# Kernel tuning notes

Measured on AMD Instinct MI355X. Metric: run time of the kernel, lower is better.

## Reference

```python
import jax, jax.numpy as jnp
import numpy as np

N_FP = 235336   # n_fingerprint
N_WORD = 7844   # n_word
D = 10          # embed / hidden dim (hard-coded in module)
K = 23          # conv kernel 2*11+1
PAD = 11
N_ATOMS = 4096
L_WORDS = 65536


def setup_inputs() -> dict:
    key = jax.random.key(0)
    ks = jax.random.split(key, 16)
    s = 0.1  # weight init scale
    return {
        "fingerprints": jax.random.randint(ks[0], (N_ATOMS,), 0, N_FP),
        # scale adjacency so x + A@hs stays O(1) over 3 layers
        "adjacency": jax.random.uniform(ks[1], (N_ATOMS, N_ATOMS), dtype=jnp.float32) * (1.0 / N_ATOMS),
        "words": jax.random.randint(ks[2], (L_WORDS,), 0, N_WORD),
        "embed_fp": jax.random.normal(ks[3], (N_FP, D), dtype=jnp.float32) * s,
        "embed_word": jax.random.normal(ks[4], (N_WORD, D), dtype=jnp.float32) * s,
        "W_gnn_w": jax.random.normal(ks[5], (3, D, D), dtype=jnp.float32) * s,
        "W_gnn_b": jax.random.normal(ks[6], (3, D), dtype=jnp.float32) * s,
        "W_cnn_w": jax.random.normal(ks[7], (3, 1, 1, K, K), dtype=jnp.float32) * (s / K),
        "W_cnn_b": jax.random.normal(ks[8], (3,), dtype=jnp.float32) * s,
        "W_att_w": jax.random.normal(ks[9], (D, D), dtype=jnp.float32) * s,
        "W_att_b": jax.random.normal(ks[10], (D,), dtype=jnp.float32) * s,
        "W_out_w": jax.random.normal(ks[11], (3, 2 * D, 2 * D), dtype=jnp.float32) * s,
        "W_out_b": jax.random.normal(ks[12], (3, 2 * D), dtype=jnp.float32) * s,
        "W_int_w": jax.random.normal(ks[13], (2, 2 * D), dtype=jnp.float32) * s,
        "W_int_b": jax.random.normal(ks[14], (2,), dtype=jnp.float32) * s,
    }


def reference(fingerprints, adjacency, words, embed_fp, embed_word,
              W_gnn_w, W_gnn_b, W_cnn_w, W_cnn_b, W_att_w, W_att_b,
              W_out_w, W_out_b, W_int_w, W_int_b):
    # ---- Compound vector with GNN ----
    xs = embed_fp[fingerprints]                       # [N, D]
    for i in range(3):                                # fixed 3 layers
        hs = jax.nn.relu(xs @ W_gnn_w[i].T + W_gnn_b[i])
        xs = xs + adjacency @ hs                      # dense message passing
    compound = jnp.mean(xs, axis=0, keepdims=True)    # [1, D]

    # ---- Protein vector with attention-CNN ----
    ws = embed_word[words]                            # [L, D]
    t = ws[None, None]                                # [1,1,L,D] NCHW
    for i in range(3):
        t = jax.nn.relu(
            jax.lax.conv_general_dilated(t, W_cnn_w[i], (1, 1),
                                          [(PAD, PAD), (PAD, PAD)])
            + W_cnn_b[i])
    xs_p = t[0, 0]                                    # [L, D]

    h = jax.nn.relu(compound @ W_att_w.T + W_att_b)   # [1, D]
    hs_p = jax.nn.relu(xs_p @ W_att_w.T + W_att_b)    # [L, D]
    weights = jnp.tanh(h @ hs_p.T)                    # [1, L]
    ys = weights.T * hs_p                             # [L, D]
    protein = jnp.mean(ys, axis=0, keepdims=True)     # [1, D]

    # ---- Fusion MLP ----
    cat = jnp.concatenate([compound, protein], axis=1)  # [1, 2D]
    for j in range(3):
        cat = jax.nn.relu(cat @ W_out_w[j].T + W_out_b[j])
    return cat @ W_int_w.T + W_int_b                  # [1, 2]
```

## Files before the change

kernel.cpp:

```cpp
#include <hip/hip_runtime.h>
#include <math.h>

#define N_ATOMS 4096
#define L_WORDS 65536
#define DD 10
#define HALO 11

#define CONV_BLOCKS 256
#define CONV_BLOCK 256
#define RPW 4
#define RPB 16
#define QCOLS 1024
#define GNN_BLOCKS 1024
#define TOTAL_BLOCKS 1280
#define ATT_BLOCKS 64
#define SH_FLOATS 2926

__global__ __launch_bounds__(128) void gnn_embed(
    const int* __restrict__ fp, const float* __restrict__ embed_fp,
    const float* __restrict__ Wg, const float* __restrict__ bg,
    float* __restrict__ xs, float* __restrict__ hs)
{
    const int n = blockIdx.x * 128 + threadIdx.x;
    float x[DD];
    const float* e = embed_fp + (size_t)fp[n] * DD;
    #pragma unroll
    for (int d = 0; d < DD; ++d) x[d] = e[d];
    #pragma unroll
    for (int d = 0; d < DD; ++d) xs[d * N_ATOMS + n] = x[d];
    #pragma unroll
    for (int d = 0; d < DD; ++d) {
        float v = bg[d];
        #pragma unroll
        for (int k = 0; k < DD; ++k) v += Wg[d * DD + k] * x[k];
        hs[d * N_ATOMS + n] = fmaxf(v, 0.f);
    }
}

__global__ __launch_bounds__(128) void gnn_prep(
    const float* __restrict__ xs_in, const float* __restrict__ part,
    const float* __restrict__ Wg, const float* __restrict__ bg,
    float* __restrict__ xs_out, float* __restrict__ hs)
{
    const int n = blockIdx.x * 128 + threadIdx.x;
    float x[DD];
    #pragma unroll
    for (int d = 0; d < DD; ++d) {
        float v = xs_in[d * N_ATOMS + n];
        #pragma unroll
        for (int q = 0; q < 4; ++q)
            v += part[((size_t)q * DD + d) * N_ATOMS + n];
        x[d] = v;
        xs_out[d * N_ATOMS + n] = v;
    }
    #pragma unroll
    for (int d = 0; d < DD; ++d) {
        float v = bg[d];
        #pragma unroll
        for (int k = 0; k < DD; ++k) v += Wg[d * DD + k] * x[k];
        hs[d * N_ATOMS + n] = fmaxf(v, 0.f);
    }
}

__device__ __forceinline__ void conv_stage(
    float* sh, const int tid, const int bx,
    const float* __restrict__ tin, const int* __restrict__ words,
    const float* __restrict__ embed_word, const float* __restrict__ w,
    const float* __restrict__ bptr, float* __restrict__ tout,
    const float* __restrict__ Wa, const float* __restrict__ ba,
    float* __restrict__ hpb)
{
    const int l0 = bx * CONV_BLOCK;
    for (int idx = tid; idx < (CONV_BLOCK + 2 * HALO) * DD; idx += CONV_BLOCK) {
        int rr = idx / DD, d = idx - rr * DD;
        int gr = l0 - HALO + rr;
        float v = 0.f;
        if (gr >= 0 && gr < L_WORDS) {
            if (tin) v = tin[(size_t)gr * DD + d];
            else     v = embed_word[(size_t)words[gr] * DD + d];
        }
        sh[rr * 11 + d] = v;
    }
    __syncthreads();

    const float bias = *bptr;
    float acc[DD];
    #pragma unroll
    for (int d = 0; d < DD; ++d) acc[d] = bias;
    for (int i = 0; i < 23; ++i) {
        float row[DD];
        const float* sr = &sh[(tid + i) * 11];
        #pragma unroll
        for (int c = 0; c < DD; ++c) row[c] = sr[c];
        #pragma unroll
        for (int d = 0; d < DD; ++d) {
            #pragma unroll
            for (int c = 0; c < DD; ++c)
                acc[d] += row[c] * w[i * 23 + (c - d + 11)];
        }
    }
    const int l = l0 + tid;
    if (tout) {
        #pragma unroll
        for (int d = 0; d < DD; ++d)
            tout[(size_t)l * DD + d] = fmaxf(acc[d], 0.f);
    }
    if (hpb) {
        float xsp[DD];
        #pragma unroll
        for (int d = 0; d < DD; ++d) xsp[d] = fmaxf(acc[d], 0.f);
        #pragma unroll
        for (int d = 0; d < DD; ++d) {
            float v = ba[d];
            #pragma unroll
            for (int k = 0; k < DD; ++k) v += Wa[d * DD + k] * xsp[k];
            hpb[(size_t)l * DD + d] = fmaxf(v, 0.f);
        }
    }
}

__device__ __forceinline__ void gnn_stage(
    float* sh, const int tid, const int b,
    const float* __restrict__ hs,
    const float* __restrict__ A, float* __restrict__ part_out)
{
    const int wave = tid >> 6, lane = tid & 63;
    const int q = b & 3, rg = b >> 2;

    const int r0 = rg * RPB + wave * RPW;
    const float4* A4 = (const float4*)(A + (size_t)r0 * N_ATOMS) + q * (QCOLS / 4);
    const float4* h4 = (const float4*)hs + q * (QCOLS / 4);

    float acc[RPW][DD];
    #pragma unroll
    for (int r = 0; r < RPW; ++r)
        #pragma unroll
        for (int d = 0; d < DD; ++d) acc[r][d] = 0.f;

    #pragma unroll 1
    for (int it = 0; it < 4; ++it) {
        const int cb = it * 64 + lane;
        float4 a[RPW];
        #pragma unroll
        for (int r = 0; r < RPW; ++r) a[r] = A4[r * (N_ATOMS / 4) + cb];
        #pragma unroll
        for (int d = 0; d < DD; ++d) {
            float4 h = h4[d * (N_ATOMS / 4) + cb];
            #pragma unroll
            for (int r = 0; r < RPW; ++r) {
                acc[r][d] += a[r].x * h.x;
                acc[r][d] += a[r].y * h.y;
                acc[r][d] += a[r].z * h.z;
                acc[r][d] += a[r].w * h.w;
            }
        }
    }

    #pragma unroll
    for (int m = 1; m <= 4; m <<= 1) {
        #pragma unroll
        for (int r = 0; r < RPW; ++r)
            #pragma unroll
            for (int d = 0; d < DD; ++d)
                acc[r][d] += __shfl_xor(acc[r][d], m, 64);
    }

    if ((lane & 7) == 0) {
        const int g = lane >> 3;
        float* dst = &sh[(wave * 8 + g) * 40];
        #pragma unroll
        for (int r = 0; r < RPW; ++r)
            #pragma unroll
            for (int d = 0; d < DD; ++d) dst[r * DD + d] = acc[r][d];
    }
    __syncthreads();

    float* pdst = part_out + (size_t)q * DD * N_ATOMS + (size_t)rg * RPB;
    for (int o = tid; o < RPB * DD; o += 256) {
        const int d = o >> 4, rr = o & 15;
        const int w8 = rr >> 2, r = rr & 3;
        float v = 0.f;
        #pragma unroll
        for (int g = 0; g < 8; ++g) v += sh[(w8 * 8 + g) * 40 + r * DD + d];
        pdst[d * N_ATOMS + rr] = v;
    }
}

__global__ __launch_bounds__(256, 5) void fused_layer(
    const float* __restrict__ A, const float* __restrict__ hs,
    float* __restrict__ part_out,
    const float* __restrict__ tin, const int* __restrict__ words,
    const float* __restrict__ emb_w, const float* __restrict__ wc,
    const float* __restrict__ bc, float* __restrict__ tout,
    const float* __restrict__ Wa, const float* __restrict__ ba,
    float* __restrict__ hpb)
{
    __shared__ float sh[SH_FLOATS];
    const int tid = threadIdx.x;
    if (blockIdx.x < CONV_BLOCKS)
        conv_stage(sh, tid, blockIdx.x, tin, words, emb_w, wc, bc, tout,
                   Wa, ba, hpb);
    else
        gnn_stage(sh, tid, blockIdx.x - CONV_BLOCKS, hs, A, part_out);
}

__global__ __launch_bounds__(1024) void attn_final(
    const float* __restrict__ xs2, const float* __restrict__ part2,
    const float* __restrict__ hpb,
    const float* __restrict__ Wa, const float* __restrict__ ba,
    const float* __restrict__ Wo, const float* __restrict__ bo,
    const float* __restrict__ Wi, const float* __restrict__ bi,
    float* att_part, unsigned int* ticket, float* __restrict__ out)
{
    __shared__ float red[16][DD];
    __shared__ float shc[DD];
    __shared__ float cat[20];
    __shared__ int islast;
    const int tid = threadIdx.x, wave = tid >> 6, lane = tid & 63;

    float c[DD];
    #pragma unroll
    for (int d = 0; d < DD; ++d) c[d] = 0.f;
    #pragma unroll
    for (int s = 0; s < 4; ++s) {
        const int n = s * 1024 + tid;
        #pragma unroll
        for (int d = 0; d < DD; ++d) {
            float v = xs2[d * N_ATOMS + n];
            #pragma unroll
            for (int qq = 0; qq < 4; ++qq)
                v += part2[((size_t)qq * DD + d) * N_ATOMS + n];
            c[d] += v;
        }
    }
    #pragma unroll
    for (int m = 32; m >= 1; m >>= 1) {
        #pragma unroll
        for (int d = 0; d < DD; ++d) c[d] += __shfl_xor(c[d], m, 64);
    }
    if (lane == 0) {
        #pragma unroll
        for (int d = 0; d < DD; ++d) red[wave][d] = c[d];
    }
    __syncthreads();
    if (tid < DD) {
        float v = 0.f;
        #pragma unroll
        for (int w = 0; w < 16; ++w) v += red[w][tid];
        shc[tid] = v * (1.f / N_ATOMS);
    }
    __syncthreads();

    float h[DD];
    #pragma unroll
    for (int d = 0; d < DD; ++d) {
        float v = ba[d];
        #pragma unroll
        for (int k = 0; k < DD; ++k) v += Wa[d * DD + k] * shc[k];
        h[d] = fmaxf(v, 0.f);
    }
    const int w_ = blockIdx.x * 1024 + tid;
    float hp[DD], dotv = 0.f;
    #pragma unroll
    for (int d = 0; d < DD; ++d) {
        hp[d] = hpb[(size_t)w_ * DD + d];
        dotv += h[d] * hp[d];
    }
    const float wgt = tanhf(dotv);
    float y[DD];
    #pragma unroll
    for (int d = 0; d < DD; ++d) y[d] = wgt * hp[d];
    #pragma unroll
    for (int m = 32; m >= 1; m >>= 1) {
        #pragma unroll
        for (int d = 0; d < DD; ++d) y[d] += __shfl_xor(y[d], m, 64);
    }
    __syncthreads();
    if (lane == 0) {
        #pragma unroll
        for (int d = 0; d < DD; ++d) red[wave][d] = y[d];
    }
    __syncthreads();
    if (tid < DD) {
        float v = 0.f;
        #pragma unroll
        for (int w = 0; w < 16; ++w) v += red[w][tid];
        __hip_atomic_store(att_part + blockIdx.x * DD + tid, v,
                           __ATOMIC_RELAXED, __HIP_MEMORY_SCOPE_AGENT);
    }
    __syncthreads();

    if (tid == 0) {
        unsigned prev = __hip_atomic_fetch_add(ticket, 1u, __ATOMIC_RELAXED,
                                               __HIP_MEMORY_SCOPE_AGENT);
        islast = (prev == ATT_BLOCKS - 1);
    }
    __syncthreads();
    if (!islast) return;
    asm volatile("" ::: "memory");

    float a[DD];
    #pragma unroll
    for (int d = 0; d < DD; ++d) a[d] = 0.f;
    if (tid < ATT_BLOCKS) {
        #pragma unroll
        for (int d = 0; d < DD; ++d)
            a[d] = __hip_atomic_load(att_part + tid * DD + d,
                                     __ATOMIC_RELAXED, __HIP_MEMORY_SCOPE_AGENT);
    }
    if (wave == 0) {
        #pragma unroll
        for (int m = 32; m >= 1; m >>= 1) {
            #pragma unroll
            for (int d = 0; d < DD; ++d) a[d] += __shfl_xor(a[d], m, 64);
        }
    }
    if (tid == 0) {
        #pragma unroll
        for (int d = 0; d < DD; ++d) cat[DD + d] = a[d] * (1.f / L_WORDS);
    }
    if (tid < DD) cat[tid] = shc[tid];
    __syncthreads();
    for (int j = 0; j < 3; ++j) {
        float v = 0.f;
        if (tid < 20) {
            v = bo[j * 20 + tid];
            for (int k = 0; k < 20; ++k) v += Wo[j * 400 + tid * 20 + k] * cat[k];
        }
        __syncthreads();
        if (tid < 20) cat[tid] = fmaxf(v, 0.f);
        __syncthreads();
    }
    if (tid < 2) {
        float v = bi[tid];
        for (int k = 0; k < 20; ++k) v += Wi[tid * 20 + k] * cat[k];
        out[tid] = v;
    }
}

extern "C" void kernel_launch(void* const* d_in, const int* in_sizes, int n_in,
                              void* d_out, int out_size, void* d_ws, size_t ws_size,
                              hipStream_t stream)
{
    const int*   fp     = (const int*)d_in[0];
    const float* A      = (const float*)d_in[1];
    const int*   words  = (const int*)d_in[2];
    const float* emb_fp = (const float*)d_in[3];
    const float* emb_w  = (const float*)d_in[4];
    const float* Wg     = (const float*)d_in[5];
    const float* bg     = (const float*)d_in[6];
    const float* Wc     = (const float*)d_in[7];
    const float* bc     = (const float*)d_in[8];
    const float* Wa     = (const float*)d_in[9];
    const float* ba     = (const float*)d_in[10];
    const float* Wo     = (const float*)d_in[11];
    const float* bo     = (const float*)d_in[12];
    const float* Wi     = (const float*)d_in[13];
    const float* bi     = (const float*)d_in[14];
    float* out = (float*)d_out;
    float* ws  = (float*)d_ws;

    float* xs0   = ws;
    float* xs1   = ws + 40960;
    float* xs2   = ws + 81920;
    float* hs0   = ws + 122880;
    float* hs1   = ws + 163840;
    float* hs2   = ws + 204800;
    float* part0 = ws + 245760;
    float* part1 = ws + 409600;
    float* part2 = ws + 573440;
    float* ta    = ws + 737280;
    float* tb    = ws + 1392640;
    float* hpb   = ta;
    float* att_part = ws + 2048000;
    unsigned int* ticket = (unsigned int*)(ws + 2048640);

    hipMemsetAsync(ticket, 0, sizeof(unsigned int), stream);

    gnn_embed<<<N_ATOMS / 128, 128, 0, stream>>>(fp, emb_fp, Wg, bg, xs0, hs0);

    fused_layer<<<TOTAL_BLOCKS, 256, 0, stream>>>(
        A, hs0, part0,
        nullptr, words, emb_w, Wc, bc, ta, nullptr, nullptr, nullptr);

    gnn_prep<<<N_ATOMS / 128, 128, 0, stream>>>(
        xs0, part0, Wg + 100, bg + 10, xs1, hs1);

    fused_layer<<<TOTAL_BLOCKS, 256, 0, stream>>>(
        A, hs1, part1,
        ta, words, emb_w, Wc + 529, bc + 1, tb, nullptr, nullptr, nullptr);

    gnn_prep<<<N_ATOMS / 128, 128, 0, stream>>>(
        xs1, part1, Wg + 200, bg + 20, xs2, hs2);

    fused_layer<<<TOTAL_BLOCKS, 256, 0, stream>>>(
        A, hs2, part2,
        tb, words, emb_w, Wc + 1058, bc + 2, nullptr, Wa, ba, hpb);

    attn_final<<<ATT_BLOCKS, 1024, 0, stream>>>(
        xs2, part2, hpb, Wa, ba, Wo, bo, Wi, bi, att_part, ticket, out);
}
```

Measured before the change: 213.4 us.

## Split compound reduction into separate kernel and widen attention grid

Before this change, each of the 64 attention blocks redundantly re-reduced the whole compound vector (xs2 plus four partial sums). That work now runs once in a new 16-block comp_reduce kernel that writes per-block partials, and attn_final runs 256 blocks of 256 threads that each read those 16 partials. The GNN inner loop is also fully unrolled and the fused_layer occupancy hint is lowered from 5 to 4 blocks per CU. The trade-off is one extra kernel launch and a change in register pressure and occupancy for the main layer kernel.

```diff
diff --git a/kernel.cpp b/kernel.cpp
--- a/kernel.cpp
+++ b/kernel.cpp
@@ -13,7 +13,7 @@
 #define QCOLS 1024
 #define GNN_BLOCKS 1024
 #define TOTAL_BLOCKS 1280
-#define ATT_BLOCKS 64
+#define ATT_BLOCKS 256
 #define SH_FLOATS 2926
 
 __global__ __launch_bounds__(128) void gnn_embed(
@@ -137,7 +137,7 @@
         #pragma unroll
         for (int d = 0; d < DD; ++d) acc[r][d] = 0.f;
 
-    #pragma unroll 1
+    #pragma unroll
     for (int it = 0; it < 4; ++it) {
         const int cb = it * 64 + lane;
         float4 a[RPW];
@@ -186,7 +186,7 @@
     }
 }
 
-__global__ __launch_bounds__(256, 5) void fused_layer(
+__global__ __launch_bounds__(256, 4) void fused_layer(
     const float* __restrict__ A, const float* __restrict__ hs,
     float* __restrict__ part_out,
     const float* __restrict__ tin, const int* __restrict__ words,
@@ -204,50 +204,55 @@
         gnn_stage(sh, tid, blockIdx.x - CONV_BLOCKS, hs, A, part_out);
 }
 
-__global__ __launch_bounds__(1024) void attn_final(
-    const float* __restrict__ xs2, const float* __restrict__ part2,
-    const float* __restrict__ hpb,
+__global__ __launch_bounds__(256) void comp_reduce(
+    const float* __restrict__ xs, const float* __restrict__ p2,
+    float* __restrict__ comp_part)
+{
+    const int tid = threadIdx.x, wave = tid >> 6, lane = tid & 63;
+    const int n = blockIdx.x * 256 + tid;
+    float x[DD];
+    #pragma unroll
+    for (int d = 0; d < DD; ++d) {
+        float v = xs[d * N_ATOMS + n];
+        #pragma unroll
+        for (int qq = 0; qq < 4; ++qq)
+            v += p2[((size_t)qq * DD + d) * N_ATOMS + n];
+        x[d] = v;
+    }
+    #pragma unroll
+    for (int m = 32; m >= 1; m >>= 1) {
+        #pragma unroll
+        for (int d = 0; d < DD; ++d) x[d] += __shfl_xor(x[d], m, 64);
+    }
+    __shared__ float s[4][DD];
+    if (lane == 0) {
+        #pragma unroll
+        for (int d = 0; d < DD; ++d) s[wave][d] = x[d];
+    }
+    __syncthreads();
+    if (tid < DD)
+        comp_part[blockIdx.x * DD + tid] =
+            s[0][tid] + s[1][tid] + s[2][tid] + s[3][tid];
+}
+
+__global__ __launch_bounds__(256) void attn_final(
+    const float* __restrict__ comp_part, const float* __restrict__ hpb,
     const float* __restrict__ Wa, const float* __restrict__ ba,
     const float* __restrict__ Wo, const float* __restrict__ bo,
     const float* __restrict__ Wi, const float* __restrict__ bi,
     float* att_part, unsigned int* ticket, float* __restrict__ out)
 {
-    __shared__ float red[16][DD];
+    __shared__ float red[4][DD];
     __shared__ float shc[DD];
     __shared__ float cat[20];
     __shared__ int islast;
     const int tid = threadIdx.x, wave = tid >> 6, lane = tid & 63;
 
-    float c[DD];
-    #pragma unroll
-    for (int d = 0; d < DD; ++d) c[d] = 0.f;
-    #pragma unroll
-    for (int s = 0; s < 4; ++s) {
-        const int n = s * 1024 + tid;
-        #pragma unroll
-        for (int d = 0; d < DD; ++d) {
-            float v = xs2[d * N_ATOMS + n];
-            #pragma unroll
-            for (int qq = 0; qq < 4; ++qq)
-                v += part2[((size_t)qq * DD + d) * N_ATOMS + n];
-            c[d] += v;
-        }
-    }
-    #pragma unroll
-    for (int m = 32; m >= 1; m >>= 1) {
-        #pragma unroll
-        for (int d = 0; d < DD; ++d) c[d] += __shfl_xor(c[d], m, 64);
-    }
-    if (lane == 0) {
-        #pragma unroll
-        for (int d = 0; d < DD; ++d) red[wave][d] = c[d];
-    }
-    __syncthreads();
     if (tid < DD) {
-        float v = 0.f;
-        #pragma unroll
-        for (int w = 0; w < 16; ++w) v += red[w][tid];
-        shc[tid] = v * (1.f / N_ATOMS);
+        float c = 0.f;
+        #pragma unroll
+        for (int p = 0; p < 16; ++p) c += comp_part[p * DD + tid];
+        shc[tid] = c * (1.f / N_ATOMS);
     }
     __syncthreads();
 
@@ -259,7 +264,7 @@
         for (int k = 0; k < DD; ++k) v += Wa[d * DD + k] * shc[k];
         h[d] = fmaxf(v, 0.f);
     }
-    const int w_ = blockIdx.x * 1024 + tid;
+    const int w_ = blockIdx.x * 256 + tid;
     float hp[DD], dotv = 0.f;
     #pragma unroll
     for (int d = 0; d < DD; ++d) {
@@ -275,16 +280,13 @@
         #pragma unroll
         for (int d = 0; d < DD; ++d) y[d] += __shfl_xor(y[d], m, 64);
     }
-    __syncthreads();
     if (lane == 0) {
         #pragma unroll
         for (int d = 0; d < DD; ++d) red[wave][d] = y[d];
     }
     __syncthreads();
     if (tid < DD) {
-        float v = 0.f;
-        #pragma unroll
-        for (int w = 0; w < 16; ++w) v += red[w][tid];
+        float v = red[0][tid] + red[1][tid] + red[2][tid] + red[3][tid];
         __hip_atomic_store(att_part + blockIdx.x * DD + tid, v,
                            __ATOMIC_RELAXED, __HIP_MEMORY_SCOPE_AGENT);
     }
@@ -301,25 +303,25 @@
 
     float a[DD];
     #pragma unroll
-    for (int d = 0; d < DD; ++d) a[d] = 0.f;
-    if (tid < ATT_BLOCKS) {
-        #pragma unroll
-        for (int d = 0; d < DD; ++d)
-            a[d] = __hip_atomic_load(att_part + tid * DD + d,
-                                     __ATOMIC_RELAXED, __HIP_MEMORY_SCOPE_AGENT);
-    }
-    if (wave == 0) {
-        #pragma unroll
-        for (int m = 32; m >= 1; m >>= 1) {
-            #pragma unroll
-            for (int d = 0; d < DD; ++d) a[d] += __shfl_xor(a[d], m, 64);
-        }
-    }
-    if (tid == 0) {
-        #pragma unroll
-        for (int d = 0; d < DD; ++d) cat[DD + d] = a[d] * (1.f / L_WORDS);
-    }
-    if (tid < DD) cat[tid] = shc[tid];
+    for (int d = 0; d < DD; ++d)
+        a[d] = __hip_atomic_load(att_part + tid * DD + d,
+                                 __ATOMIC_RELAXED, __HIP_MEMORY_SCOPE_AGENT);
+    #pragma unroll
+    for (int m = 32; m >= 1; m >>= 1) {
+        #pragma unroll
+        for (int d = 0; d < DD; ++d) a[d] += __shfl_xor(a[d], m, 64);
+    }
+    __syncthreads();
+    if (lane == 0) {
+        #pragma unroll
+        for (int d = 0; d < DD; ++d) red[wave][d] = a[d];
+    }
+    __syncthreads();
+    if (tid < DD) {
+        float pv = red[0][tid] + red[1][tid] + red[2][tid] + red[3][tid];
+        cat[DD + tid] = pv * (1.f / L_WORDS);
+        cat[tid] = shc[tid];
+    }
     __syncthreads();
     for (int j = 0; j < 3; ++j) {
         float v = 0.f;
@@ -372,8 +374,9 @@
     float* ta    = ws + 737280;
     float* tb    = ws + 1392640;
     float* hpb   = ta;
-    float* att_part = ws + 2048000;
-    unsigned int* ticket = (unsigned int*)(ws + 2048640);
+    float* att_part  = ws + 2048000;
+    float* comp_part = ws + 2050560;
+    unsigned int* ticket = (unsigned int*)(ws + 2050720);
 
     hipMemsetAsync(ticket, 0, sizeof(unsigned int), stream);
 
@@ -397,6 +400,8 @@
         A, hs2, part2,
         tb, words, emb_w, Wc + 1058, bc + 2, nullptr, Wa, ba, hpb);
 
-    attn_final<<<ATT_BLOCKS, 1024, 0, stream>>>(
-        xs2, part2, hpb, Wa, ba, Wo, bo, Wi, bi, att_part, ticket, out);
-}
+    comp_reduce<<<16, 256, 0, stream>>>(xs2, part2, comp_part);
+
+    attn_final<<<ATT_BLOCKS, 256, 0, stream>>>(
+        comp_part, hpb, Wa, ba, Wo, bo, Wi, bi, att_part, ticket, out);
+}
```

Result: faster. 208.3 us (-2.4%).
